# Kernel tuning notes

Measured on AMD Instinct MI355X. Metric: run time of the kernel, lower is better.

The kernel has to match this reference:

```python
import jax, jax.numpy as jnp
import numpy as np

N_NODES = 50000


def _gcn_conv(x, row, col, W, b, n_nodes):
    """PyG GCNConv: symmetric-normalized scatter-add aggregation.
    row/col already include self-loops. x: [N, Fin], W: [Fin, Fout]."""
    h = x @ W  # [N, Fout]
    deg = jax.ops.segment_sum(jnp.ones(col.shape[0], x.dtype), col,
                              num_segments=n_nodes)  # in-degree incl. self-loops
    dis = jnp.where(deg > 0, jax.lax.rsqrt(deg), 0.0)  # deg^{-1/2}
    norm = dis[row] * dis[col]  # [E+N]
    msg = h[row] * norm[:, None]  # gather + scale, [E+N, Fout]
    out = jax.ops.segment_sum(msg, col, num_segments=n_nodes)  # scatter-add
    return out + b


def setup_inputs() -> dict:
    key = jax.random.key(0)
    k1, k2, k3, k4 = jax.random.split(key, 4)
    N, E, FIN, FH = N_NODES, 800000, 512, 512
    x = jax.random.normal(k1, (N, FIN), dtype=jnp.float32)
    edge_index = jax.random.randint(k2, (2, E), 0, N, dtype=jnp.int64)
    W1 = jax.random.normal(k3, (FIN, FH), dtype=jnp.float32) * (1.0 / np.sqrt(FIN))
    b1 = jnp.zeros((FH,), jnp.float32)
    W2 = jax.random.normal(k4, (FH, FH), dtype=jnp.float32) * (1.0 / np.sqrt(FH))
    b2 = jnp.zeros((FH,), jnp.float32)
    return {"x": x, "edge_index": edge_index, "W1": W1, "b1": b1,
            "W2": W2, "b2": b2}


def reference(x, edge_index, W1, b1, W2, b2):
    n = x.shape[0]
    loops = jnp.arange(n, dtype=edge_index.dtype)
    row = jnp.concatenate([edge_index[0], loops])  # sources
    col = jnp.concatenate([edge_index[1], loops])  # targets
    h = _gcn_conv(x, row, col, W1, b1, n)
    h = jax.nn.relu(h)
    return _gcn_conv(h, row, col, W2, b2, n)
```

## Files before the change

### kernel.cpp

```cpp
#include <hip/hip_runtime.h>
#include <hip/hip_bf16.h>

typedef short short8 __attribute__((ext_vector_type(8)));
typedef unsigned short u16x8 __attribute__((ext_vector_type(8)));
typedef float f32x4 __attribute__((ext_vector_type(4)));

#define AS1 __attribute__((address_space(1)))
#define AS3 __attribute__((address_space(3)))

__device__ __forceinline__ void gload16(const void* g, void* l) {
  __builtin_amdgcn_global_load_lds((AS1 void*)g, (AS3 void*)l, 16, 0, 0);
}

__device__ __forceinline__ unsigned short f2bf(float f) {
  unsigned u = __float_as_uint(f);
  u = (u + 0x7FFF + ((u >> 16) & 1)) >> 16;
  return (unsigned short)u;
}
__device__ __forceinline__ float bf2f(unsigned short u) {
  return __uint_as_float(((unsigned)u) << 16);
}

__global__ void prep_kernel(const float4* __restrict__ x4, ushort4* __restrict__ xb4, int n4,
                            const float* __restrict__ W1, unsigned short* __restrict__ W1t,
                            const float* __restrict__ W2, unsigned short* __restrict__ W2t) {
  const int nthr = gridDim.x * 256;
  for (int i = blockIdx.x * 256 + threadIdx.x; i < n4; i += nthr) {
    float4 v = x4[i];
    ushort4 o;
    o.x = f2bf(v.x); o.y = f2bf(v.y); o.z = f2bf(v.z); o.w = f2bf(v.w);
    xb4[i] = o;
  }
  for (int idx = blockIdx.x * 256 + threadIdx.x; idx < 512 * 512; idx += nthr) {
    const int k = idx >> 9, n = idx & 511;
    W1t[n * 512 + k] = f2bf(W1[idx]);
    W2t[n * 512 + k] = f2bf(W2[idx]);
  }
}

__global__ void detect64_kernel(const int* __restrict__ ei32, int* __restrict__ flag) {
  if (blockIdx.x == 0 && threadIdx.x == 0) {
    int f = 1;
    for (int i = 0; i < 64; ++i)
      if (ei32[2 * i + 1] != 0) { f = 0; break; }
    *flag = f;
  }
}

__global__ void count_kernel(const int* __restrict__ ei32, const int* __restrict__ flag,
                             int* __restrict__ cnt, int E) {
  int e = blockIdx.x * 256 + threadIdx.x;
  if (e >= E) return;
  int c = (*flag) ? ei32[2 * E + 2 * e] : ei32[E + e];
  atomicAdd(&cnt[c], 1);
}

__global__ void __launch_bounds__(1024) scan_bsum_kernel(const int* __restrict__ cnt,
                                                         int* __restrict__ bsum, int n) {
  __shared__ int ws[16];
  const int tid = threadIdx.x, lane = tid & 63, wid = tid >> 6;
  const int i = blockIdx.x * 1024 + tid;
  int x = (i < n) ? cnt[i] : 0;
#pragma unroll
  for (int d = 1; d < 64; d <<= 1) x += __shfl_xor(x, d, 64);
  if (lane == 0) ws[wid] = x;
  __syncthreads();
  if (tid == 0) {
    int s = 0;
#pragma unroll
    for (int w = 0; w < 16; ++w) s += ws[w];
    bsum[blockIdx.x] = s;
  }
}

__global__ void scan_boff_kernel(int* __restrict__ bsum, int* __restrict__ total, int B) {
  const int lane = threadIdx.x;
  const int v = (lane < B) ? bsum[lane] : 0;
  int x = v;
#pragma unroll
  for (int d = 1; d < 64; d <<= 1) {
    int y = __shfl_up(x, d, 64);
    if (lane >= d) x += y;
  }
  if (lane < B) bsum[lane] = x - v;
  if (lane == B - 1) *total = x;
}

__global__ void __launch_bounds__(1024) scan_fill_kernel(const int* __restrict__ cnt,
    const int* __restrict__ boff, int* __restrict__ ptr, int* __restrict__ cur,
    float* __restrict__ dis, int n) {
  __shared__ int ws[16];
  const int tid = threadIdx.x, lane = tid & 63, wid = tid >> 6;
  const int i = blockIdx.x * 1024 + tid;
  const int v = (i < n) ? cnt[i] : 0;
  int x = v;
#pragma unroll
  for (int d = 1; d < 64; d <<= 1) {
    int y = __shfl_up(x, d, 64);
    if (lane >= d) x += y;
  }
  if (lane == 63) ws[wid] = x;
  __syncthreads();
  if (tid < 16) {
    int wv = ws[tid];
    int wx = wv;
#pragma unroll
    for (int d = 1; d < 16; d <<= 1) {
      int y = __shfl_up(wx, d, 64);
      if (tid >= d) wx += y;
    }
    ws[tid] = wx - wv;
  }
  __syncthreads();
  if (i < n) {
    const int excl = boff[blockIdx.x] + ws[wid] + (x - v);
    ptr[i] = excl;
    cur[i] = excl;
    dis[i] = rsqrtf((float)(v + 1));
  }
}

__global__ void fill_kernel(const int* __restrict__ ei32, const int* __restrict__ flag,
                            int* __restrict__ cur, int* __restrict__ eidx, int E) {
  int e = blockIdx.x * 256 + threadIdx.x;
  if (e >= E) return;
  int is64 = *flag;
  int r = is64 ? ei32[2 * e] : ei32[e];
  int c = is64 ? ei32[2 * E + 2 * e] : ei32[E + e];
  int pos = atomicAdd(&cur[c], 1);
  eidx[pos] = r;
}

template <bool BA, bool BC>
__global__ void __launch_bounds__(256) gemm_kernel(const unsigned short* __restrict__ A,
                                                   const unsigned short* __restrict__ Bt,
                                                   const float* __restrict__ dscale,
                                                   unsigned short* __restrict__ C, int M) {
  __shared__ alignas(128) unsigned short As[2][8192];
  __shared__ alignas(128) unsigned short Bs[2][8192];
  const int tid = threadIdx.x;
  const int wave = tid >> 6, lane = tid & 63;
  const int wm = wave >> 1, wn = wave & 1;

  const int nbm = (M + 127) >> 7;
  const int nwg = nbm * 4;
  const int orig = blockIdx.x;
  const int xcd = orig & 7;
  const int q8 = nwg >> 3, r8 = nwg & 7;
  const int wg = (xcd < r8 ? xcd * (q8 + 1) : r8 * (q8 + 1) + (xcd - r8) * q8) + (orig >> 3);
  const int bn = wg & 3;
  const int bm = wg >> 2;

  const int lr = lane >> 3, ls = lane & 7;
  const int fr = lane & 15, ks = lane >> 4;

  f32x4 acc[4][4] = {};

#define STAGE(BUF, KO)                                                                     \
  {                                                                                        \
    _Pragma("unroll") for (int i = 0; i < 4; ++i) {                                        \
      int ra = bm * 128 + i * 32 + wave * 8 + lr;                                          \
      ra = ra < M ? ra : M - 1;                                                            \
      const size_t aoff = BA ? ((size_t)(KO)*M + (size_t)ra * 64 + ((ls ^ (lr & 7)) << 3)) \
                             : ((size_t)ra * 512 + (KO) + ((ls ^ (lr & 7)) << 3));         \
      gload16(A + aoff, &As[BUF][(i * 32 + wave * 8) * 64]);                               \
      const int rb = bn * 128 + i * 32 + wave * 8 + lr;                                    \
      gload16(Bt + (size_t)rb * 512 + (KO) + ((ls ^ (lr & 7)) << 3),                       \
              &Bs[BUF][(i * 32 + wave * 8) * 64]);                                         \
    }                                                                                      \
  }

  STAGE(0, 0)
  __syncthreads();

  int buf = 0;
  for (int kt = 0; kt < 8; ++kt) {
    if (kt < 7) STAGE(buf ^ 1, (kt + 1) * 64)

    short8 af[2][4], bfg[2][4];
#pragma unroll
    for (int m = 0; m < 4; ++m) {
      const int tr = wm * 64 + m * 16 + fr;
      af[0][m] = *(const short8*)&As[buf][tr * 64 + (((ks * 8)      ) ^ ((tr & 7) << 3))];
      af[1][m] = *(const short8*)&As[buf][tr * 64 + (((ks * 8) + 32 ) ^ ((tr & 7) << 3))];
    }
#pragma unroll
    for (int n = 0; n < 4; ++n) {
      const int tb = wn * 64 + n * 16 + fr;
      bfg[0][n] = *(const short8*)&Bs[buf][tb * 64 + (((ks * 8)      ) ^ ((tb & 7) << 3))];
      bfg[1][n] = *(const short8*)&Bs[buf][tb * 64 + (((ks * 8) + 32 ) ^ ((tb & 7) << 3))];
    }
#pragma unroll
    for (int kk = 0; kk < 2; ++kk)
#pragma unroll
      for (int m = 0; m < 4; ++m)
#pragma unroll
        for (int n = 0; n < 4; ++n)
          acc[m][n] = __builtin_amdgcn_mfma_f32_16x16x32_bf16(af[kk][m], bfg[kk][n], acc[m][n], 0, 0, 0);

    __syncthreads();
    buf ^= 1;
  }
#undef STAGE

  const int rbase = bm * 128 + wm * 64 + (lane >> 4) * 4;
  const int cbase = bn * 128 + wn * 64 + (lane & 15);
  const size_t hseg = (size_t)M * 64;
#pragma unroll
  for (int m = 0; m < 4; ++m)
#pragma unroll
    for (int j = 0; j < 4; ++j) {
      const int r = rbase + m * 16 + j;
      if (r < M) {
        const float ds = dscale[r];
#pragma unroll
        for (int n = 0; n < 4; ++n) {
          const unsigned short val = f2bf(acc[m][n][j] * ds);
          if (BC) {
            const int col = cbase + n * 16;
            C[(size_t)(col >> 6) * hseg + (size_t)r * 64 + (col & 63)] = val;
          } else {
            C[(size_t)r * 512 + cbase + n * 16] = val;
          }
        }
      }
    }
}

template <bool FINAL>
__global__ void __launch_bounds__(256) agg_kernel(const unsigned short* __restrict__ h,
    const int* __restrict__ eidx, const int* __restrict__ ptr, const float* __restrict__ dis,
    const float* __restrict__ bias, void* __restrict__ outv, int n) {
  const int tid = threadIdx.x;
  const int lane = tid & 63;
  const int slice = blockIdx.x & 7;
  const int g = lane >> 3;
  const int c = lane & 7;
  const int node = (int)(blockIdx.x >> 3) * 32 + (tid >> 6) * 8 + g;
  if (node >= n) return;

  const unsigned short* hs = h + (size_t)slice * ((size_t)n * 64);
  const int coff = c * 8;

  const int start = ptr[node], end = ptr[node + 1];
  float acc[8] = {0, 0, 0, 0, 0, 0, 0, 0};

  int e = start;
  for (; e + 2 <= end; e += 2) {
    const int s0 = eidx[e], s1 = eidx[e + 1];
    const u16x8 v0 = *(const u16x8*)(hs + (size_t)(unsigned)s0 * 64 + coff);
    const u16x8 v1 = *(const u16x8*)(hs + (size_t)(unsigned)s1 * 64 + coff);
#pragma unroll
    for (int j = 0; j < 8; ++j) acc[j] += bf2f(v0[j]) + bf2f(v1[j]);
  }
  if (e < end) {
    const int s0 = eidx[e];
    const u16x8 v = *(const u16x8*)(hs + (size_t)(unsigned)s0 * 64 + coff);
#pragma unroll
    for (int j = 0; j < 8; ++j) acc[j] += bf2f(v[j]);
  }

  {
    const u16x8 v = *(const u16x8*)(hs + (size_t)node * 64 + coff);
#pragma unroll
    for (int j = 0; j < 8; ++j) acc[j] += bf2f(v[j]);
  }

  const float di = dis[node];
  const int fcol = slice * 64 + coff;
  float b[8];
  *(float4*)&b[0] = *(const float4*)(bias + fcol);
  *(float4*)&b[4] = *(const float4*)(bias + fcol + 4);

  if (FINAL) {
    float* out = (float*)outv;
    float4 o0, o1;
    o0.x = acc[0] * di + b[0]; o0.y = acc[1] * di + b[1];
    o0.z = acc[2] * di + b[2]; o0.w = acc[3] * di + b[3];
    o1.x = acc[4] * di + b[4]; o1.y = acc[5] * di + b[5];
    o1.z = acc[6] * di + b[6]; o1.w = acc[7] * di + b[7];
    *(float4*)(out + (size_t)node * 512 + fcol) = o0;
    *(float4*)(out + (size_t)node * 512 + fcol + 4) = o1;
  } else {
    unsigned short* out = (unsigned short*)outv;
    u16x8 o;
#pragma unroll
    for (int j = 0; j < 8; ++j) {
      const float t = acc[j] * di + b[j];
      o[j] = f2bf(t > 0.0f ? t : 0.0f);
    }
    *(u16x8*)(out + (size_t)slice * ((size_t)n * 64) + (size_t)node * 64 + coff) = o;
  }
}

extern "C" void kernel_launch(void* const* d_in, const int* in_sizes, int n_in,
                              void* d_out, int out_size, void* d_ws, size_t ws_size,
                              hipStream_t stream) {
  const float* x  = (const float*)d_in[0];
  const int*   ei = (const int*)d_in[1];
  const float* W1 = (const float*)d_in[2];
  const float* b1 = (const float*)d_in[3];
  const float* W2 = (const float*)d_in[4];
  const float* b2 = (const float*)d_in[5];
  float* out = (float*)d_out;

  const int M = in_sizes[0] / 512;
  const int E = in_sizes[1] / 2;

  auto alignup = [](size_t v) { return (v + 255) & ~(size_t)255; };
  char* p = (char*)d_ws;
  unsigned short* xb  = (unsigned short*)p; p += alignup((size_t)M * 512 * 2);
  unsigned short* h1b = (unsigned short*)p; p += alignup((size_t)M * 512 * 2);
  unsigned short* r1b = (unsigned short*)p; p += alignup((size_t)M * 512 * 2);
  unsigned short* w1b = (unsigned short*)p; p += alignup(512 * 512 * 2);
  unsigned short* w2b = (unsigned short*)p; p += alignup(512 * 512 * 2);
  float* dis = (float*)p; p += alignup((size_t)M * 4);
  int* ptr   = (int*)p;   p += alignup((size_t)(M + 1) * 4);
  int* cur   = (int*)p;   p += alignup((size_t)M * 4);
  int* eidx  = (int*)p;   p += alignup((size_t)E * 4);
  int* flag  = (int*)p;   p += alignup(256);
  int* bsum  = (int*)p;   p += alignup(1024);
  int* cnt = (int*)h1b;
  unsigned short* h2b = xb;

  hipMemsetAsync(cnt, 0, (size_t)M * 4, stream);
  detect64_kernel<<<1, 64, 0, stream>>>(ei, flag);

  prep_kernel<<<2048, 256, 0, stream>>>((const float4*)x, (ushort4*)xb, M * 128,
                                        W1, w1b, W2, w2b);

  const int B = (M + 1023) / 1024;
  count_kernel<<<(E + 255) / 256, 256, 0, stream>>>(ei, flag, cnt, E);
  scan_bsum_kernel<<<B, 1024, 0, stream>>>(cnt, bsum, M);
  scan_boff_kernel<<<1, 64, 0, stream>>>(bsum, ptr + M, B);
  scan_fill_kernel<<<B, 1024, 0, stream>>>(cnt, bsum, ptr, cur, dis, M);
  fill_kernel<<<(E + 255) / 256, 256, 0, stream>>>(ei, flag, cur, eidx, E);

  const int nwg = ((M + 127) / 128) * 4;
  const int nag = ((M + 31) / 32) * 8;
  gemm_kernel<false, true><<<nwg, 256, 0, stream>>>(xb, w1b, dis, h1b, M);
  agg_kernel<false><<<nag, 256, 0, stream>>>(h1b, eidx, ptr, dis, b1, (void*)r1b, M);
  gemm_kernel<true, true><<<nwg, 256, 0, stream>>>(r1b, w2b, dis, h2b, M);
  agg_kernel<true><<<nag, 256, 0, stream>>>(h2b, eidx, ptr, dis, b2, (void*)out, M);
}
```

Before: 410.9 us.

## Stage GEMM epilogue through LDS for coalesced 16-byte stores

After: 417.5 us. About the same (+1.6%).

```diff
diff --git a/kernel.cpp b/kernel.cpp
--- a/kernel.cpp
+++ b/kernel.cpp
@@ -39,12 +39,10 @@
 }
 
 __global__ void detect64_kernel(const int* __restrict__ ei32, int* __restrict__ flag) {
-  if (blockIdx.x == 0 && threadIdx.x == 0) {
-    int f = 1;
-    for (int i = 0; i < 64; ++i)
-      if (ei32[2 * i + 1] != 0) { f = 0; break; }
-    *flag = f;
-  }
+  const int lane = threadIdx.x;
+  const int v = ei32[2 * lane + 1];
+  const unsigned long long m = __ballot(v != 0);
+  if (lane == 0) *flag = (m == 0ull) ? 1 : 0;
 }
 
 __global__ void count_kernel(const int* __restrict__ ei32, const int* __restrict__ flag,
@@ -132,10 +130,10 @@
 }
 
 template <bool BA, bool BC>
-__global__ void __launch_bounds__(256) gemm_kernel(const unsigned short* __restrict__ A,
-                                                   const unsigned short* __restrict__ Bt,
-                                                   const float* __restrict__ dscale,
-                                                   unsigned short* __restrict__ C, int M) {
+__global__ void __launch_bounds__(256, 2) gemm_kernel(const unsigned short* __restrict__ A,
+                                                      const unsigned short* __restrict__ Bt,
+                                                      const float* __restrict__ dscale,
+                                                      unsigned short* __restrict__ C, int M) {
   __shared__ alignas(128) unsigned short As[2][8192];
   __shared__ alignas(128) unsigned short Bs[2][8192];
   const int tid = threadIdx.x;
@@ -203,28 +201,47 @@
   }
 #undef STAGE
 
-  const int rbase = bm * 128 + wm * 64 + (lane >> 4) * 4;
-  const int cbase = bn * 128 + wn * 64 + (lane & 15);
-  const size_t hseg = (size_t)M * 64;
+  unsigned short (*EP)[128] = (unsigned short(*)[128])&As[0][0];
+  const int rb0 = wm * 64 + (lane >> 4) * 4;
+  const int cb0 = wn * 64 + (lane & 15);
 #pragma unroll
   for (int m = 0; m < 4; ++m)
 #pragma unroll
     for (int j = 0; j < 4; ++j) {
-      const int r = rbase + m * 16 + j;
-      if (r < M) {
-        const float ds = dscale[r];
-#pragma unroll
-        for (int n = 0; n < 4; ++n) {
-          const unsigned short val = f2bf(acc[m][n][j] * ds);
-          if (BC) {
-            const int col = cbase + n * 16;
-            C[(size_t)(col >> 6) * hseg + (size_t)r * 64 + (col & 63)] = val;
-          } else {
-            C[(size_t)r * 512 + cbase + n * 16] = val;
-          }
-        }
+      const int row = rb0 + m * 16 + j;
+      int rg = bm * 128 + row;
+      rg = rg < M ? rg : M - 1;
+      const float ds = dscale[rg];
+#pragma unroll
+      for (int n = 0; n < 4; ++n) {
+        const int col = cb0 + n * 16;
+        EP[row][(((col >> 3) ^ (row & 7)) << 3) + (col & 7)] = f2bf(acc[m][n][j] * ds);
       }
     }
+  __syncthreads();
+
+  {
+    const int r = tid >> 1, hf = tid & 1;
+    const int R = bm * 128 + r;
+    if (R < M) {
+      u16x8 v[8];
+#pragma unroll
+      for (int i = 0; i < 8; ++i) {
+        const int slot = hf * 8 + (i ^ (r & 7));
+        v[i] = *(const u16x8*)&EP[r][slot << 3];
+      }
+      if (BC) {
+        const size_t hseg = (size_t)M * 64;
+        unsigned short* dst = C + (size_t)(bn * 2 + hf) * hseg + (size_t)R * 64;
+#pragma unroll
+        for (int i = 0; i < 8; ++i) *(u16x8*)(dst + i * 8) = v[i];
+      } else {
+        unsigned short* dst = C + (size_t)R * 512 + bn * 128 + hf * 64;
+#pragma unroll
+        for (int i = 0; i < 8; ++i) *(u16x8*)(dst + i * 8) = v[i];
+      }
+    }
+  }
 }
 
 template <bool FINAL>
```

## Bucket CSR edges by source quarter to improve gather locality

Applied to the files above, without the earlier changes.

After: 404.8 us. No clear change (-1.5%).

```diff
diff --git a/kernel.cpp b/kernel.cpp
--- a/kernel.cpp
+++ b/kernel.cpp
@@ -39,20 +39,21 @@
 }
 
 __global__ void detect64_kernel(const int* __restrict__ ei32, int* __restrict__ flag) {
-  if (blockIdx.x == 0 && threadIdx.x == 0) {
-    int f = 1;
-    for (int i = 0; i < 64; ++i)
-      if (ei32[2 * i + 1] != 0) { f = 0; break; }
-    *flag = f;
-  }
+  const int lane = threadIdx.x;
+  const int v = ei32[2 * lane + 1];
+  const unsigned long long m = __ballot(v != 0);
+  if (lane == 0) *flag = (m == 0ull) ? 1 : 0;
 }
 
 __global__ void count_kernel(const int* __restrict__ ei32, const int* __restrict__ flag,
-                             int* __restrict__ cnt, int E) {
+                             int* __restrict__ cnt4, int E, int qdiv) {
   int e = blockIdx.x * 256 + threadIdx.x;
   if (e >= E) return;
-  int c = (*flag) ? ei32[2 * E + 2 * e] : ei32[E + e];
-  atomicAdd(&cnt[c], 1);
+  const int is64 = *flag;
+  const int r = is64 ? ei32[2 * e] : ei32[e];
+  const int c = is64 ? ei32[2 * E + 2 * e] : ei32[E + e];
+  int q = r / qdiv; q = q > 3 ? 3 : q;
+  atomicAdd(&cnt4[c * 4 + q], 1);
 }
 
 __global__ void __launch_bounds__(1024) scan_bsum_kernel(const int* __restrict__ cnt,
@@ -73,17 +74,33 @@
   }
 }
 
-__global__ void scan_boff_kernel(int* __restrict__ bsum, int* __restrict__ total, int B) {
-  const int lane = threadIdx.x;
-  const int v = (lane < B) ? bsum[lane] : 0;
+__global__ void __launch_bounds__(1024) scan_boff_kernel(int* __restrict__ bsum,
+                                                         int* __restrict__ total, int B) {
+  __shared__ int ws[16];
+  const int tid = threadIdx.x, lane = tid & 63, wid = tid >> 6;
+  const int v = (tid < B) ? bsum[tid] : 0;
   int x = v;
 #pragma unroll
   for (int d = 1; d < 64; d <<= 1) {
     int y = __shfl_up(x, d, 64);
     if (lane >= d) x += y;
   }
-  if (lane < B) bsum[lane] = x - v;
-  if (lane == B - 1) *total = x;
+  if (lane == 63) ws[wid] = x;
+  __syncthreads();
+  if (tid < 16) {
+    int wv = ws[tid];
+    int wx = wv;
+#pragma unroll
+    for (int d = 1; d < 16; d <<= 1) {
+      int y = __shfl_up(wx, d, 64);
+      if (tid >= d) wx += y;
+    }
+    ws[tid] = wx - wv;
+  }
+  __syncthreads();
+  const int excl = ws[wid] + (x - v);
+  if (tid < B) bsum[tid] = excl;
+  if (tid == B - 1) *total = excl + v;
 }
 
 __global__ void __launch_bounds__(1024) scan_fill_kernel(const int* __restrict__ cnt,
@@ -91,8 +108,8 @@
     float* __restrict__ dis, int n) {
   __shared__ int ws[16];
   const int tid = threadIdx.x, lane = tid & 63, wid = tid >> 6;
-  const int i = blockIdx.x * 1024 + tid;
-  const int v = (i < n) ? cnt[i] : 0;
+  const int j = blockIdx.x * 1024 + tid;
+  const int v = (j < n) ? cnt[j] : 0;
   int x = v;
 #pragma unroll
   for (int d = 1; d < 64; d <<= 1) {
@@ -112,22 +129,26 @@
     ws[tid] = wx - wv;
   }
   __syncthreads();
-  if (i < n) {
+  const int v1 = __shfl_down(v, 1, 64);
+  const int v2 = __shfl_down(v, 2, 64);
+  const int v3 = __shfl_down(v, 3, 64);
+  if (j < n) {
     const int excl = boff[blockIdx.x] + ws[wid] + (x - v);
-    ptr[i] = excl;
-    cur[i] = excl;
-    dis[i] = rsqrtf((float)(v + 1));
+    ptr[j] = excl;
+    cur[j] = excl;
+    if ((j & 3) == 0) dis[j >> 2] = rsqrtf((float)(v + v1 + v2 + v3 + 1));
   }
 }
 
 __global__ void fill_kernel(const int* __restrict__ ei32, const int* __restrict__ flag,
-                            int* __restrict__ cur, int* __restrict__ eidx, int E) {
+                            int* __restrict__ cur4, int* __restrict__ eidx, int E, int qdiv) {
   int e = blockIdx.x * 256 + threadIdx.x;
   if (e >= E) return;
-  int is64 = *flag;
-  int r = is64 ? ei32[2 * e] : ei32[e];
-  int c = is64 ? ei32[2 * E + 2 * e] : ei32[E + e];
-  int pos = atomicAdd(&cur[c], 1);
+  const int is64 = *flag;
+  const int r = is64 ? ei32[2 * e] : ei32[e];
+  const int c = is64 ? ei32[2 * E + 2 * e] : ei32[E + e];
+  int q = r / qdiv; q = q > 3 ? 3 : q;
+  const int pos = atomicAdd(&cur4[c * 4 + q], 1);
   eidx[pos] = r;
 }
 
@@ -229,7 +250,7 @@
 
 template <bool FINAL>
 __global__ void __launch_bounds__(256) agg_kernel(const unsigned short* __restrict__ h,
-    const int* __restrict__ eidx, const int* __restrict__ ptr, const float* __restrict__ dis,
+    const int* __restrict__ eidx, const int* __restrict__ ptr4, const float* __restrict__ dis,
     const float* __restrict__ bias, void* __restrict__ outv, int n) {
   const int tid = threadIdx.x;
   const int lane = tid & 63;
@@ -242,7 +263,7 @@
   const unsigned short* hs = h + (size_t)slice * ((size_t)n * 64);
   const int coff = c * 8;
 
-  const int start = ptr[node], end = ptr[node + 1];
+  const int start = ptr4[node * 4], end = ptr4[node * 4 + 4];
   float acc[8] = {0, 0, 0, 0, 0, 0, 0, 0};
 
   int e = start;
@@ -306,6 +327,7 @@
 
   const int M = in_sizes[0] / 512;
   const int E = in_sizes[1] / 2;
+  const int qdiv = (M + 3) >> 2;
 
   auto alignup = [](size_t v) { return (v + 255) & ~(size_t)255; };
   char* p = (char*)d_ws;
@@ -315,31 +337,32 @@
   unsigned short* w1b = (unsigned short*)p; p += alignup(512 * 512 * 2);
   unsigned short* w2b = (unsigned short*)p; p += alignup(512 * 512 * 2);
   float* dis = (float*)p; p += alignup((size_t)M * 4);
-  int* ptr   = (int*)p;   p += alignup((size_t)(M + 1) * 4);
-  int* cur   = (int*)p;   p += alignup((size_t)M * 4);
+  int* ptr4  = (int*)p;   p += alignup(((size_t)M * 4 + 1) * 4);
   int* eidx  = (int*)p;   p += alignup((size_t)E * 4);
   int* flag  = (int*)p;   p += alignup(256);
   int* bsum  = (int*)p;   p += alignup(1024);
-  int* cnt = (int*)h1b;
+  int* cnt4 = (int*)h1b;
+  int* cur4 = (int*)((char*)h1b + alignup((size_t)M * 16));
   unsigned short* h2b = xb;
 
-  hipMemsetAsync(cnt, 0, (size_t)M * 4, stream);
+  const int n4 = M * 4;
+  hipMemsetAsync(cnt4, 0, (size_t)n4 * 4, stream);
   detect64_kernel<<<1, 64, 0, stream>>>(ei, flag);
 
   prep_kernel<<<2048, 256, 0, stream>>>((const float4*)x, (ushort4*)xb, M * 128,
                                         W1, w1b, W2, w2b);
 
-  const int B = (M + 1023) / 1024;
-  count_kernel<<<(E + 255) / 256, 256, 0, stream>>>(ei, flag, cnt, E);
-  scan_bsum_kernel<<<B, 1024, 0, stream>>>(cnt, bsum, M);
-  scan_boff_kernel<<<1, 64, 0, stream>>>(bsum, ptr + M, B);
-  scan_fill_kernel<<<B, 1024, 0, stream>>>(cnt, bsum, ptr, cur, dis, M);
-  fill_kernel<<<(E + 255) / 256, 256, 0, stream>>>(ei, flag, cur, eidx, E);
+  const int B = (n4 + 1023) / 1024;
+  count_kernel<<<(E + 255) / 256, 256, 0, stream>>>(ei, flag, cnt4, E, qdiv);
+  scan_bsum_kernel<<<B, 1024, 0, stream>>>(cnt4, bsum, n4);
+  scan_boff_kernel<<<1, 1024, 0, stream>>>(bsum, ptr4 + n4, B);
+  scan_fill_kernel<<<B, 1024, 0, stream>>>(cnt4, bsum, ptr4, cur4, dis, n4);
+  fill_kernel<<<(E + 255) / 256, 256, 0, stream>>>(ei, flag, cur4, eidx, E, qdiv);
 
   const int nwg = ((M + 127) / 128) * 4;
   const int nag = ((M + 31) / 32) * 8;
   gemm_kernel<false, true><<<nwg, 256, 0, stream>>>(xb, w1b, dis, h1b, M);
-  agg_kernel<false><<<nag, 256, 0, stream>>>(h1b, eidx, ptr, dis, b1, (void*)r1b, M);
+  agg_kernel<false><<<nag, 256, 0, stream>>>(h1b, eidx, ptr4, dis, b1, (void*)r1b, M);
   gemm_kernel<true, true><<<nwg, 256, 0, stream>>>(r1b, w2b, dis, h2b, M);
-  agg_kernel<true><<<nag, 256, 0, stream>>>(h2b, eidx, ptr, dis, b2, (void*)out, M);
-}
+  agg_kernel<true><<<nag, 256, 0, stream>>>(h2b, eidx, ptr4, dis, b2, (void*)out, M);
+}
```
